# Optimization experiments

Hardware: AMD Instinct MI355X
Metric: run time of the kernel (lower is better)

Reference implementation:

```python
import jax, jax.numpy as jnp
import numpy as np

B, T, D, H = 16, 1024, 512, 8
DH = D // H
NEG = jnp.float32(-2**32 + 1)


def setup_inputs() -> dict:
    key = jax.random.key(0)
    ks = jax.random.split(key, 9)
    s = 1.0 / np.sqrt(D)
    return {
        "queries": jax.random.normal(ks[0], (B, T, D), jnp.float32),
        "keys": jax.random.normal(ks[1], (B, T, D), jnp.float32),
        "value": jax.random.normal(ks[2], (B, T, D), jnp.float32),
        "Wq": jax.random.normal(ks[3], (D, D), jnp.float32) * s,
        "bq": jnp.zeros((D,), jnp.float32),
        "Wk": jax.random.normal(ks[4], (D, D), jnp.float32) * s,
        "bk": jnp.zeros((D,), jnp.float32),
        "Wv": jax.random.normal(ks[5], (D, D), jnp.float32) * s,
        "bv": jnp.zeros((D,), jnp.float32),
    }


def reference(queries, keys, value, Wq, bq, Wk, bk, Wv, bv):
    b, tq, d = queries.shape
    tk = keys.shape[1]
    # linear projections
    Q = queries @ Wq + bq   # [B,Tq,D]
    K = keys @ Wk + bk      # [B,Tk,D]
    V = value @ Wv + bv     # [B,Tk,D]
    # split heads: chunk along feature dim == reshape to [B,T,H,DH]
    Qh = Q.reshape(b, tq, H, DH)
    Kh = K.reshape(b, tk, H, DH)
    Vh = V.reshape(b, tk, H, DH)
    scores = jnp.einsum("bqhd,bkhd->bhqk", Qh, Kh) / jnp.sqrt(jnp.float32(DH))
    # key padding mask: rows of keys summing to 0 are padding
    key_mask = jnp.sign(jnp.abs(keys.sum(axis=-1)))      # [B,Tk]
    scores = jnp.where(key_mask[:, None, None, :] == 0, NEG, scores)
    # causal mask
    causal = jnp.tril(jnp.ones((tq, tk), jnp.float32))   # [Tq,Tk]
    scores = jnp.where(causal[None, None, :, :] == 0, NEG, scores)
    probs = jax.nn.softmax(scores, axis=-1)              # [B,H,Tq,Tk]
    # query padding mask (applied AFTER softmax, as in source)
    query_mask = jnp.sign(jnp.abs(queries.sum(axis=-1)))  # [B,Tq]
    probs = probs * query_mask[:, None, :, None]
    # dropout_rate=0.0 -> identity
    out = jnp.einsum("bhqk,bkhd->bqhd", probs, Vh).reshape(b, tq, d)
    return out + queries  # residual
```

## Files before the change

kernel.cpp:

```cpp
#include <hip/hip_runtime.h>
#include <hip/hip_bf16.h>

#define B_ 16
#define T_ 1024
#define D_ 512
#define H_ 8
#define M_ (B_ * T_)

typedef __attribute__((ext_vector_type(4))) float f32x4;
typedef __attribute__((ext_vector_type(8))) short bf16x8;
typedef __attribute__((ext_vector_type(4))) short bf16x4;

__device__ __forceinline__ void gld_lds16(const void* g, void* l) {
    __builtin_amdgcn_global_load_lds((const __attribute__((address_space(1))) void*)g,
                                     (__attribute__((address_space(3))) void*)l, 16, 0, 0);
}

__device__ __forceinline__ short f2bf(float f) {
    union { float f; unsigned u; } v; v.f = f;
    unsigned r = v.u + 0x7FFF + ((v.u >> 16) & 1);
    return (short)(r >> 16);
}

__global__ void wtrans_kernel(const float* __restrict__ Wq, const float* __restrict__ Wk,
                              const float* __restrict__ Wv, short* __restrict__ WtAll) {
    __shared__ float tile[64][65];
    const int t = threadIdx.x;
    const int mat = blockIdx.y;
    const float* W = (mat == 0) ? Wq : (mat == 1) ? Wk : Wv;
    short* Wt = WtAll + (size_t)mat * D_ * D_;
    const int kt = (blockIdx.x >> 3) * 64;
    const int nt = (blockIdx.x & 7) * 64;
#pragma unroll
    for (int i = 0; i < 4; ++i) {
        int idx = t + i * 256;
        int r = idx >> 4, c4 = idx & 15;
        float4 v = *(const float4*)&W[(kt + r) * D_ + nt + c4 * 4];
        tile[r][c4 * 4 + 0] = v.x; tile[r][c4 * 4 + 1] = v.y;
        tile[r][c4 * 4 + 2] = v.z; tile[r][c4 * 4 + 3] = v.w;
    }
    __syncthreads();
#pragma unroll
    for (int i = 0; i < 2; ++i) {
        int idx = t + i * 256;
        int nr = idx >> 3, c8 = idx & 7;
        bf16x8 pk;
#pragma unroll
        for (int j = 0; j < 8; ++j) pk[j] = f2bf(tile[c8 * 8 + j][nr]);
        *(bf16x8*)&Wt[(nt + nr) * D_ + kt + c8 * 8] = pk;
    }
}

__global__ void cvt_mask_kernel(const float* __restrict__ q, const float* __restrict__ k,
                                const float* __restrict__ v, short* __restrict__ Xbf,
                                float* __restrict__ qm, float* __restrict__ kb) {
    const int w = threadIdx.x >> 6, lane = threadIdx.x & 63;
    const int which = blockIdx.y;
    const int row = blockIdx.x * 4 + w;
    const float* X = (which == 0) ? q : (which == 1) ? k : v;
    short* O = Xbf + (size_t)which * M_ * D_;
    const float4* p = (const float4*)&X[(size_t)row * D_];
    float4 v0 = p[lane], v1 = p[lane + 64];
    float s = v0.x + v0.y + v0.z + v0.w + v1.x + v1.y + v1.z + v1.w;
#pragma unroll
    for (int m = 1; m < 64; m <<= 1) s += __shfl_xor(s, m);
    bf16x4 p0, p1;
    p0[0] = f2bf(v0.x); p0[1] = f2bf(v0.y); p0[2] = f2bf(v0.z); p0[3] = f2bf(v0.w);
    p1[0] = f2bf(v1.x); p1[1] = f2bf(v1.y); p1[2] = f2bf(v1.z); p1[3] = f2bf(v1.w);
    *(bf16x4*)&O[(size_t)row * D_ + lane * 4] = p0;
    *(bf16x4*)&O[(size_t)row * D_ + 256 + lane * 4] = p1;
    if (lane == 0) {
        if (which == 0) qm[row] = (s != 0.0f) ? 1.0f : 0.0f;
        else if (which == 1) kb[row] = (s != 0.0f) ? 0.0f : -3e30f;
    }
}

__global__ __launch_bounds__(256) void proj_gemm_bf(
    const short* __restrict__ Xbf, const short* __restrict__ WtAll,
    const float* __restrict__ bq, const float* __restrict__ bk, const float* __restrict__ bv,
    short* __restrict__ QKV) {
    __shared__ char As[16384];
    __shared__ char Bs[16384];
    const int t = threadIdx.x;
    const int mat = blockIdx.z;
    const short* X  = Xbf + (size_t)mat * M_ * D_;
    const short* Wt = WtAll + (size_t)mat * D_ * D_;
    const float* bias = (mat == 0) ? bq : (mat == 1) ? bk : bv;
    short* dst = QKV + (size_t)mat * M_ * D_;
    const int n0 = blockIdx.x * 128, m0 = blockIdx.y * 128;
    const int lane = t & 63, w = t >> 6;
    const int wr = w >> 1, wc = w & 1;
    const int cl = lane & 15, g = lane >> 4;

    const int r0 = t >> 3, c0 = ((t & 7) ^ (r0 & 7)) * 8;
    const short* sA = X  + (size_t)(m0 + r0) * D_ + c0;
    const short* sB = Wt + (size_t)(n0 + r0) * D_ + c0;

    f32x4 acc[4][4] = {};
#pragma unroll
    for (int i = 0; i < 4; ++i) {
        gld_lds16(sA + (size_t)(32 * i) * D_, As + t * 16 + i * 4096);
        gld_lds16(sB + (size_t)(32 * i) * D_, Bs + t * 16 + i * 4096);
    }
    for (int kt = 0; kt < D_; kt += 64) {
        __syncthreads();
#pragma unroll
        for (int ks = 0; ks < 2; ++ks) {
            bf16x8 a[4], b[4];
#pragma unroll
            for (int m = 0; m < 4; ++m)
                a[m] = *(const bf16x8*)(As + (wr * 64 + m * 16 + cl) * 128 + (((ks * 4 + g) ^ (cl & 7)) << 4));
#pragma unroll
            for (int n = 0; n < 4; ++n)
                b[n] = *(const bf16x8*)(Bs + (wc * 64 + n * 16 + cl) * 128 + (((ks * 4 + g) ^ (cl & 7)) << 4));
#pragma unroll
            for (int m = 0; m < 4; ++m)
#pragma unroll
                for (int n = 0; n < 4; ++n)
                    acc[m][n] = __builtin_amdgcn_mfma_f32_16x16x32_bf16(a[m], b[n], acc[m][n], 0, 0, 0);
        }
        __syncthreads();
        if (kt + 64 < D_) {
            const int k2 = kt + 64;
#pragma unroll
            for (int i = 0; i < 4; ++i) {
                gld_lds16(sA + (size_t)(32 * i) * D_ + k2, As + t * 16 + i * 4096);
                gld_lds16(sB + (size_t)(32 * i) * D_ + k2, Bs + t * 16 + i * 4096);
            }
        }
    }
#pragma unroll
    for (int n = 0; n < 4; ++n) {
        int col = n0 + wc * 64 + n * 16 + cl;
        float bv2 = bias[col];
#pragma unroll
        for (int m = 0; m < 4; ++m) {
            int rowb = m0 + wr * 64 + m * 16 + g * 4;
#pragma unroll
            for (int j = 0; j < 4; ++j)
                dst[(size_t)(rowb + j) * D_ + col] = f2bf(acc[m][n][j] + bv2);
        }
    }
}

__global__ __launch_bounds__(256) void proj_gemm(
    const float* __restrict__ Xq, const float* __restrict__ Xk, const float* __restrict__ Xv,
    const short* __restrict__ WtAll,
    const float* __restrict__ bq, const float* __restrict__ bk, const float* __restrict__ bv,
    short* __restrict__ Qb, short* __restrict__ Kb, short* __restrict__ Vb) {
    __shared__ short As2[128][72];
    __shared__ short Bs2[128][72];
    const int t = threadIdx.x;
    const int mat = blockIdx.z;
    const float* X = (mat == 0) ? Xq : (mat == 1) ? Xk : Xv;
    const short* Wt = WtAll + (size_t)mat * D_ * D_;
    const float* bias = (mat == 0) ? bq : (mat == 1) ? bk : bv;
    short* dst = (mat == 0) ? Qb : (mat == 1) ? Kb : Vb;
    const int m0 = blockIdx.x * 128, n0 = blockIdx.y * 128;
    const int lane = t & 63, w = t >> 6;
    const int wr = w >> 1, wc = w & 1;
    const int cl = lane & 15, g = lane >> 4;
    f32x4 acc[4][4] = {};
    for (int kt = 0; kt < D_; kt += 64) {
#pragma unroll
        for (int i = 0; i < 8; ++i) {
            int idx = t + 256 * i;
            int r = idx >> 4, c4 = idx & 15;
            float4 v = *(const float4*)&X[(size_t)(m0 + r) * D_ + kt + c4 * 4];
            bf16x4 pk;
            pk[0] = f2bf(v.x); pk[1] = f2bf(v.y); pk[2] = f2bf(v.z); pk[3] = f2bf(v.w);
            *(bf16x4*)&As2[r][c4 * 4] = pk;
        }
#pragma unroll
        for (int i = 0; i < 4; ++i) {
            int idx = t + 256 * i;
            int r = idx >> 3, c8 = idx & 7;
            *(bf16x8*)&Bs2[r][c8 * 8] = *(const bf16x8*)&Wt[(size_t)(n0 + r) * D_ + kt + c8 * 8];
        }
        __syncthreads();
#pragma unroll
        for (int ks = 0; ks < 2; ++ks) {
            bf16x8 a[4], b[4];
#pragma unroll
            for (int m = 0; m < 4; ++m)
                a[m] = *(const bf16x8*)&As2[wr * 64 + m * 16 + cl][ks * 32 + g * 8];
#pragma unroll
            for (int n = 0; n < 4; ++n)
                b[n] = *(const bf16x8*)&Bs2[wc * 64 + n * 16 + cl][ks * 32 + g * 8];
#pragma unroll
            for (int m = 0; m < 4; ++m)
#pragma unroll
                for (int n = 0; n < 4; ++n)
                    acc[m][n] = __builtin_amdgcn_mfma_f32_16x16x32_bf16(a[m], b[n], acc[m][n], 0, 0, 0);
        }
        __syncthreads();
    }
#pragma unroll
    for (int n = 0; n < 4; ++n) {
        int col = n0 + wc * 64 + n * 16 + cl;
        float bv2 = bias[col];
#pragma unroll
        for (int m = 0; m < 4; ++m) {
            int rowb = m0 + wr * 64 + m * 16 + g * 4;
#pragma unroll
            for (int j = 0; j < 4; ++j)
                dst[(size_t)(rowb + j) * D_ + col] = f2bf(acc[m][n][j] + bv2);
        }
    }
}

__global__ void mask_kernel(const float* __restrict__ queries, const float* __restrict__ keys,
                            float* __restrict__ qm, float* __restrict__ kb) {
    const int w = threadIdx.x >> 6, lane = threadIdx.x & 63;
    const int row = blockIdx.x * 4 + w;
    const int which = blockIdx.y;
    const float* X = which ? keys : queries;
    const float4* p = (const float4*)&X[(size_t)row * D_];
    float s = 0.f;
#pragma unroll
    for (int i = 0; i < 2; ++i) {
        float4 v = p[lane + 64 * i];
        s += v.x + v.y + v.z + v.w;
    }
#pragma unroll
    for (int m = 1; m < 64; m <<= 1) s += __shfl_xor(s, m);
    if (lane == 0) {
        if (which) kb[row] = (s != 0.0f) ? 0.0f : -3e30f;
        else       qm[row] = (s != 0.0f) ? 1.0f : 0.0f;
    }
}

__global__ void vtrans_kernel(const short* __restrict__ Vb, short* __restrict__ VtG) {
    __shared__ short tile[64][72];
    const int t = threadIdx.x;
    const int kt = blockIdx.x & 15;
    const int h  = (blockIdx.x >> 4) & 7;
    const int b  = blockIdx.x >> 7;
#pragma unroll
    for (int i = 0; i < 2; ++i) {
        int idx = t + i * 256;
        int r = idx >> 3, c8 = idx & 7;
        *(bf16x8*)&tile[((r & 7) << 3) | (r >> 3)][c8 * 8] =
            *(const bf16x8*)&Vb[(size_t)(b * T_ + kt * 64 + r) * D_ + h * 64 + c8 * 8];
    }
    __syncthreads();
#pragma unroll
    for (int i = 0; i < 2; ++i) {
        int idx = t + i * 256;
        int d = idx >> 3, r8 = idx & 7;
        bf16x8 pk;
#pragma unroll
        for (int j = 0; j < 8; ++j) pk[j] = tile[(j << 3) | r8][d];
        *(bf16x8*)&VtG[(size_t)((b * 8 + h) * 64 + d) * T_ + kt * 64 + r8 * 8] = pk;
    }
}

__device__ __forceinline__ void qk_mfma(f32x4 (&s)[4], const char* Kl,
                                        const bf16x8 (&q)[2], int cl, int g) {
#pragma unroll
    for (int kc = 0; kc < 2; ++kc)
#pragma unroll
        for (int nc = 0; nc < 4; ++nc) {
            bf16x8 a = *(const bf16x8*)(Kl + (nc * 16 + cl) * 128 + (((kc * 4 + g) ^ (cl & 7)) << 4));
            s[nc] = __builtin_amdgcn_mfma_f32_16x16x32_bf16(a, q[kc], s[nc], 0, 0, 0);
        }
}

template <bool CAUSAL>
__device__ __forceinline__ void smax_pv(f32x4 (&s)[4], const f32x4 (&kb4)[4],
                                        f32x4 (&o)[4], float& m, float& l,
                                        int qmk, const char* Vl, int cl, int g) {
    const float csc = 0.125f * 1.44269504088896f;
    float pm = -3e30f;
#pragma unroll
    for (int nc = 0; nc < 4; ++nc)
#pragma unroll
        for (int j = 0; j < 4; ++j) {
            float v = fmaf(s[nc][j], csc, kb4[nc][j]);
            if (CAUSAL && (nc * 16 + g * 4 + j > qmk)) v = -3e30f;
            s[nc][j] = v;
            pm = fmaxf(pm, v);
        }
    pm = fmaxf(pm, __shfl_xor(pm, 16));
    pm = fmaxf(pm, __shfl_xor(pm, 32));
    if (__any(pm > m + 8.f)) {
        float mn = fmaxf(m, pm), cf;
        asm("v_exp_f32 %0, %1" : "=v"(cf) : "v"(m - mn));
        l *= cf;
        m = mn;
#pragma unroll
        for (int j = 0; j < 4; ++j) {
            float cfj = __shfl(cf, g * 4 + j);
#pragma unroll
            for (int dc = 0; dc < 4; ++dc) o[dc][j] *= cfj;
        }
    }
    float ps = 0.f;
#pragma unroll
    for (int nc = 0; nc < 4; ++nc)
#pragma unroll
        for (int j = 0; j < 4; ++j) {
            float p;
            asm("v_exp_f32 %0, %1" : "=v"(p) : "v"(s[nc][j] - m));
            s[nc][j] = p;
            ps += p;
        }
    ps += __shfl_xor(ps, 16);
    ps += __shfl_xor(ps, 32);
    l += ps;

    unsigned wp[4][2];
#pragma unroll
    for (int nc = 0; nc < 4; ++nc) {
        asm("v_cvt_pk_bf16_f32 %0, %1, %2" : "=v"(wp[nc][0]) : "v"(s[nc][0]), "v"(s[nc][1]));
        asm("v_cvt_pk_bf16_f32 %0, %1, %2" : "=v"(wp[nc][1]) : "v"(s[nc][2]), "v"(s[nc][3]));
    }
    const bool bp = (g & 1);
#pragma unroll
    for (int ks = 0; ks < 2; ++ks) {
        unsigned A0 = wp[2 * ks][0], A1 = wp[2 * ks][1];
        unsigned B0 = wp[2 * ks + 1][0], B1 = wp[2 * ks + 1][1];
        unsigned snd0 = bp ? A0 : B0, snd1 = bp ? A1 : B1;
        unsigned rcv0 = __shfl_xor(snd0, 16), rcv1 = __shfl_xor(snd1, 16);
        union { unsigned u[4]; bf16x8 v; } pa;
        pa.u[0] = bp ? rcv0 : A0;
        pa.u[1] = bp ? rcv1 : A1;
        pa.u[2] = bp ? B0 : rcv0;
        pa.u[3] = bp ? B1 : rcv1;
        const int vg = ks * 4 + (g & 1) * 2 + (g >> 1);
#pragma unroll
        for (int dc = 0; dc < 4; ++dc) {
            bf16x8 vv = *(const bf16x8*)(Vl + (dc * 16 + cl) * 128 + ((vg ^ (cl & 7)) << 4));
            o[dc] = __builtin_amdgcn_mfma_f32_16x16x32_bf16(pa.v, vv, o[dc], 0, 0, 0);
        }
    }
}

__global__ __launch_bounds__(256, 4) void attn_kernel(
    const short* __restrict__ Qb, const short* __restrict__ Kb,
    const short* __restrict__ VtG, const float* __restrict__ qmask,
    const float* __restrict__ kbias, const float* __restrict__ queries,
    float* __restrict__ out) {
    __shared__ char KV[2][2][8192];
    __shared__ float kbL[1024];
    const int t = threadIdx.x, lane = t & 63, w = t >> 6;
    const int cl = lane & 15, g = lane >> 4;
    const int u = blockIdx.x;
    const int wgid = (u & 7) * 128 + (u >> 3);
    const int pr = wgid & 7, h = (wgid >> 3) & 7, b = wgid >> 6;

    const int rS0 = t >> 3,  cS0 = ((t & 7) ^ (rS0 & 7)) * 8;
    const int t2 = t + 256;
    const int rS1 = t2 >> 3, cS1 = ((t2 & 7) ^ (rS1 & 7)) * 8;
    const short* kS0 = Kb  + ((size_t)(b * T_) + rS0) * D_ + h * 64 + cS0;
    const short* kS1 = Kb  + ((size_t)(b * T_) + rS1) * D_ + h * 64 + cS1;
    const short* vS0 = VtG + (size_t)((b * 8 + h) * 64 + rS0) * T_ + cS0;
    const short* vS1 = VtG + (size_t)((b * 8 + h) * 64 + rS1) * T_ + cS1;

    gld_lds16(kbias + b * T_ + t * 4, (char*)kbL + t * 16);

    int tb = 0;
#pragma unroll
    for (int pass = 0; pass < 2; ++pass) {
        const int qtile = pass ? pr : 15 - pr;
        const int nt = qtile + 1;
        const int qr = qtile * 64 + w * 16 + cl;

        bf16x8 qb[2];
#pragma unroll
        for (int kc = 0; kc < 2; ++kc)
            qb[kc] = *(const bf16x8*)&Qb[(size_t)(b * T_ + qr) * D_ + h * 64 + kc * 32 + g * 8];

        gld_lds16(kS0, &KV[tb][0][0]    + t * 16);
        gld_lds16(kS1, &KV[tb][0][4096] + t * 16);
        gld_lds16(vS0, &KV[tb][1][0]    + t * 16);
        gld_lds16(vS1, &KV[tb][1][4096] + t * 16);

        f32x4 o[4] = {};
        float m = -3e30f, l = 0.f;

        for (int it = 0; it < nt; ++it) {
            __syncthreads();

            f32x4 kb4[4];
#pragma unroll
            for (int nc = 0; nc < 4; ++nc)
                kb4[nc] = *(const f32x4*)((const char*)kbL + it * 256 + nc * 64 + g * 16);

            if (it + 1 < nt) {
                const int kt2 = (it + 1) * 64;
                char* db = &KV[tb ^ 1][0][0];
                gld_lds16(kS0 + (size_t)kt2 * D_, db + t * 16);
                gld_lds16(kS1 + (size_t)kt2 * D_, db + 4096 + t * 16);
                gld_lds16(vS0 + kt2, db + 8192 + t * 16);
                gld_lds16(vS1 + kt2, db + 8192 + 4096 + t * 16);
            }

            const char* Kl = &KV[tb][0][0];
            const char* Vl = &KV[tb][1][0];

            f32x4 s[4] = {};
            qk_mfma(s, Kl, qb, cl, g);
            if (it == nt - 1) smax_pv<true >(s, kb4, o, m, l, w * 16 + cl, Vl, cl, g);
            else              smax_pv<false>(s, kb4, o, m, l, 0,           Vl, cl, g);
            tb ^= 1;
        }

        float inv = 1.0f / l;
#pragma unroll
        for (int j = 0; j < 4; ++j) {
            float linv = __shfl(inv, g * 4 + j);
            const int q = qtile * 64 + w * 16 + g * 4 + j;
            const float sc2 = linv * qmask[b * T_ + q];
            const size_t base = (size_t)(b * T_ + q) * D_ + h * 64;
#pragma unroll
            for (int dc = 0; dc < 4; ++dc) {
                const size_t idx = base + dc * 16 + cl;
                out[idx] = o[dc][j] * sc2 + queries[idx];
            }
        }
    }
}

extern "C" void kernel_launch(void* const* d_in, const int* in_sizes, int n_in,
                              void* d_out, int out_size, void* d_ws, size_t ws_size,
                              hipStream_t stream) {
    const float* queries = (const float*)d_in[0];
    const float* keys    = (const float*)d_in[1];
    const float* value   = (const float*)d_in[2];
    const float* Wq      = (const float*)d_in[3];
    const float* bq      = (const float*)d_in[4];
    const float* Wk      = (const float*)d_in[5];
    const float* bk      = (const float*)d_in[6];
    const float* Wv      = (const float*)d_in[7];
    const float* bv      = (const float*)d_in[8];
    float* out = (float*)d_out;

    char* ws = (char*)d_ws;
    const size_t WT_SZ  = (size_t)D_ * D_ * 2;
    const size_t XB_SZ  = (size_t)M_ * D_ * 2;

    const size_t NEED = 3 * WT_SZ + 6 * XB_SZ + 2 * (size_t)M_ * 4;
    if (ws_size >= NEED) {
        short* WtAll = (short*)(ws);
        short* Xbf   = (short*)(ws + 3 * WT_SZ);
        short* QKV   = (short*)(ws + 3 * WT_SZ + 3 * XB_SZ);
        short* Qb = QKV, *Kb = QKV + M_ * D_, *Vb = QKV + 2 * (size_t)M_ * D_;
        short* VtG   = Xbf;
        float* qm    = (float*)(ws + 3 * WT_SZ + 6 * XB_SZ);
        float* kb    = qm + M_;

        wtrans_kernel<<<dim3(64, 3), 256, 0, stream>>>(Wq, Wk, Wv, WtAll);
        cvt_mask_kernel<<<dim3(M_ / 4, 3), 256, 0, stream>>>(queries, keys, value, Xbf, qm, kb);
        proj_gemm_bf<<<dim3(D_ / 128, M_ / 128, 3), 256, 0, stream>>>(
            Xbf, WtAll, bq, bk, bv, QKV);
        vtrans_kernel<<<B_ * H_ * (T_ / 64), 256, 0, stream>>>(Vb, VtG);
        attn_kernel<<<1024, 256, 0, stream>>>(Qb, Kb, VtG, qm, kb, queries, out);
    } else {
        short* WtAll = (short*)(ws);
        short* Qb  = (short*)(ws + 3 * WT_SZ);
        short* Kb  = (short*)(ws + 3 * WT_SZ + XB_SZ);
        short* Vb  = (short*)(ws + 3 * WT_SZ + 2 * XB_SZ);
        short* VtG = (short*)(ws + 3 * WT_SZ + 3 * XB_SZ);
        float* qm  = (float*)(ws + 3 * WT_SZ + 4 * XB_SZ);
        float* kb  = qm + M_;

        wtrans_kernel<<<dim3(64, 3), 256, 0, stream>>>(Wq, Wk, Wv, WtAll);
        mask_kernel<<<dim3(M_ / 4, 2), 256, 0, stream>>>(queries, keys, qm, kb);
        proj_gemm<<<dim3(M_ / 128, D_ / 128, 3), 256, 0, stream>>>(
            queries, keys, value, WtAll, bq, bk, bv, Qb, Kb, Vb);
        vtrans_kernel<<<B_ * H_ * (T_ / 64), 256, 0, stream>>>(Vb, VtG);
        attn_kernel<<<1024, 256, 0, stream>>>(Qb, Kb, VtG, qm, kb, queries, out);
    }
}
```

Baseline: 116.6 us.

## Fuse V transpose into projection GEMM epilogue and remap workgroups for XCD locality

The projection GEMM now writes V directly in the transposed per-head layout that attention consumes, so the separate vtrans kernel launch and its extra read and write of V are dropped when the workspace is large enough. The grid is flattened to 1D, and workgroup ids are remapped so that consecutive tiles land on the same XCD, which should improve L2 reuse of A and B tiles. The transposed store writes 4 contiguous bf16 values per lane along T, which gives less coalesced writes. It also needs one extra workspace buffer.

After: 107.3 us. 8.0% less time.

```diff
diff --git a/kernel.cpp b/kernel.cpp
--- a/kernel.cpp
+++ b/kernel.cpp
@@ -78,16 +78,19 @@
 __global__ __launch_bounds__(256) void proj_gemm_bf(
     const short* __restrict__ Xbf, const short* __restrict__ WtAll,
     const float* __restrict__ bq, const float* __restrict__ bk, const float* __restrict__ bv,
-    short* __restrict__ QKV) {
+    short* __restrict__ QKV, short* __restrict__ VtG) {
     __shared__ char As[16384];
     __shared__ char Bs[16384];
     const int t = threadIdx.x;
-    const int mat = blockIdx.z;
+    const int u = blockIdx.x;
+    const int wgid = (u & 7) * 192 + (u >> 3);
+    const int mat = wgid >> 9;
+    const int r = wgid & 511;
+    const int m0 = (r >> 2) << 7, n0 = (r & 3) << 7;
     const short* X  = Xbf + (size_t)mat * M_ * D_;
     const short* Wt = WtAll + (size_t)mat * D_ * D_;
     const float* bias = (mat == 0) ? bq : (mat == 1) ? bk : bv;
     short* dst = QKV + (size_t)mat * M_ * D_;
-    const int n0 = blockIdx.x * 128, m0 = blockIdx.y * 128;
     const int lane = t & 63, w = t >> 6;
     const int wr = w >> 1, wc = w & 1;
     const int cl = lane & 15, g = lane >> 4;
@@ -129,16 +132,35 @@
             }
         }
     }
-#pragma unroll
-    for (int n = 0; n < 4; ++n) {
-        int col = n0 + wc * 64 + n * 16 + cl;
-        float bv2 = bias[col];
-#pragma unroll
-        for (int m = 0; m < 4; ++m) {
-            int rowb = m0 + wr * 64 + m * 16 + g * 4;
-#pragma unroll
-            for (int j = 0; j < 4; ++j)
-                dst[(size_t)(rowb + j) * D_ + col] = f2bf(acc[m][n][j] + bv2);
+    if (VtG != nullptr && mat == 2) {
+        const int bb = m0 >> 10, tl0 = m0 & 1023;
+#pragma unroll
+        for (int n = 0; n < 4; ++n) {
+            const int col = n0 + wc * 64 + n * 16 + cl;
+            const int h = col >> 6, dh = col & 63;
+            short* vrow = VtG + ((size_t)(bb * 8 + h) * 64 + dh) * T_;
+            const float bv2 = bias[col];
+#pragma unroll
+            for (int m = 0; m < 4; ++m) {
+                const int tl = tl0 + wr * 64 + m * 16 + g * 4;
+                bf16x4 pk;
+#pragma unroll
+                for (int j = 0; j < 4; ++j) pk[j] = f2bf(acc[m][n][j] + bv2);
+                *(bf16x4*)&vrow[tl] = pk;
+            }
+        }
+    } else {
+#pragma unroll
+        for (int n = 0; n < 4; ++n) {
+            int col = n0 + wc * 64 + n * 16 + cl;
+            float bv2 = bias[col];
+#pragma unroll
+            for (int m = 0; m < 4; ++m) {
+                int rowb = m0 + wr * 64 + m * 16 + g * 4;
+#pragma unroll
+                for (int j = 0; j < 4; ++j)
+                    dst[(size_t)(rowb + j) * D_ + col] = f2bf(acc[m][n][j] + bv2);
+            }
         }
     }
 }
@@ -439,9 +461,25 @@
     char* ws = (char*)d_ws;
     const size_t WT_SZ  = (size_t)D_ * D_ * 2;
     const size_t XB_SZ  = (size_t)M_ * D_ * 2;
-
-    const size_t NEED = 3 * WT_SZ + 6 * XB_SZ + 2 * (size_t)M_ * 4;
-    if (ws_size >= NEED) {
+    const size_t MASKS  = 2 * (size_t)M_ * 4;
+
+    const size_t NEED_FULL = 3 * WT_SZ + 7 * XB_SZ + MASKS;
+    const size_t NEED_MID  = 3 * WT_SZ + 6 * XB_SZ + MASKS;
+
+    if (ws_size >= NEED_FULL) {
+        short* WtAll = (short*)(ws);
+        short* Xbf   = (short*)(ws + 3 * WT_SZ);
+        short* QKV   = (short*)(ws + 3 * WT_SZ + 3 * XB_SZ);
+        short* Qb = QKV, *Kb = QKV + M_ * D_;
+        short* VtG   = (short*)(ws + 3 * WT_SZ + 6 * XB_SZ);
+        float* qm    = (float*)(ws + 3 * WT_SZ + 7 * XB_SZ);
+        float* kb    = qm + M_;
+
+        wtrans_kernel<<<dim3(64, 3), 256, 0, stream>>>(Wq, Wk, Wv, WtAll);
+        cvt_mask_kernel<<<dim3(M_ / 4, 3), 256, 0, stream>>>(queries, keys, value, Xbf, qm, kb);
+        proj_gemm_bf<<<1536, 256, 0, stream>>>(Xbf, WtAll, bq, bk, bv, QKV, VtG);
+        attn_kernel<<<1024, 256, 0, stream>>>(Qb, Kb, VtG, qm, kb, queries, out);
+    } else if (ws_size >= NEED_MID) {
         short* WtAll = (short*)(ws);
         short* Xbf   = (short*)(ws + 3 * WT_SZ);
         short* QKV   = (short*)(ws + 3 * WT_SZ + 3 * XB_SZ);
@@ -452,8 +490,7 @@
 
         wtrans_kernel<<<dim3(64, 3), 256, 0, stream>>>(Wq, Wk, Wv, WtAll);
         cvt_mask_kernel<<<dim3(M_ / 4, 3), 256, 0, stream>>>(queries, keys, value, Xbf, qm, kb);
-        proj_gemm_bf<<<dim3(D_ / 128, M_ / 128, 3), 256, 0, stream>>>(
-            Xbf, WtAll, bq, bk, bv, QKV);
+        proj_gemm_bf<<<1536, 256, 0, stream>>>(Xbf, WtAll, bq, bk, bv, QKV, nullptr);
         vtrans_kernel<<<B_ * H_ * (T_ / 64), 256, 0, stream>>>(Vb, VtG);
         attn_kernel<<<1024, 256, 0, stream>>>(Qb, Kb, VtG, qm, kb, queries, out);
     } else {
```
